# Kernel optimization log

Hardware: AMD Instinct MI355X
Metric: run time of the kernel (lower is better)

## Reference

```python
import jax, jax.numpy as jnp
import numpy as np

K = 3          # kernel_size
N = K * K      # sampling points per pixel
STRIDE = 1
PAD = 1
DIL = 1


def _conv2d(x, w, b):
    # standard NCHW conv for offset / modulation branches
    y = jax.lax.conv_general_dilated(
        x, w, window_strides=(STRIDE, STRIDE),
        padding=((PAD, PAD), (PAD, PAD)),
        rhs_dilation=(DIL, DIL),
        dimension_numbers=('NCHW', 'OIHW', 'NCHW'))
    return y + b[None, :, None, None]


def setup_inputs() -> dict:
    key = jax.random.key(0)
    ks = jax.random.split(key, 6)
    B, C, H, W, O = 8, 64, 96, 96, 64
    x = jax.random.normal(ks[0], (B, C, H, W), jnp.float32)
    # small random offset/modulation weights so sampling points are off-grid
    offset_w = jax.random.normal(ks[1], (2 * N, C, K, K), jnp.float32) * 0.01
    offset_b = jax.random.normal(ks[2], (2 * N,), jnp.float32) * 0.1
    m_w = jax.random.normal(ks[3], (N, C, K, K), jnp.float32) * 0.01
    m_b = jnp.zeros((N,), jnp.float32)
    # Conv3d(in=C, out=O, kernel=(1,1,N)) weight squeezed to [O, C, N]
    conv_w = jax.random.normal(ks[4], (O, C, N), jnp.float32) * (2.0 / (C * N)) ** 0.5
    conv_b = jnp.zeros((O,), jnp.float32)
    return dict(x=x, offset_w=offset_w, offset_b=offset_b,
                m_w=m_w, m_b=m_b, conv_w=conv_w, conv_b=conv_b)


def _deform_forward(x, offset_w, offset_b, m_w, m_b, conv_w, conv_b):
    B, C, H, W = x.shape
    offset = _conv2d(x, offset_w, offset_b)           # [B, 2n, h, w]
    m = jax.nn.sigmoid(_conv2d(x, m_w, m_b))          # [B, n, h, w]
    xp = jnp.pad(x, ((0, 0), (0, 0), (PAD, PAD), (PAD, PAD)))
    Hp, Wp = xp.shape[2], xp.shape[3]
    off = jnp.transpose(offset, (0, 2, 3, 1))         # [B, h, w, 2n]
    mod = jnp.transpose(m, (0, 2, 3, 1))              # [B, h, w, n]

    # p0: conv-center grid on the padded input; pn: kernel-tap offsets
    st = ((K - 1) // 2) * DIL
    p0_x = jnp.arange(st, Hp - (K // 2) * DIL, STRIDE, dtype=jnp.float32)  # [h]
    p0_y = jnp.arange(st, Wp - (K // 2) * DIL, STRIDE, dtype=jnp.float32)  # [w]
    r = jnp.arange(-((K - 1) // 2) * DIL, (K // 2) * DIL + 1, DIL, dtype=jnp.float32)
    pn_x, pn_y = jnp.meshgrid(r, r, indexing='ij')
    pn_x, pn_y = pn_x.reshape(N), pn_y.reshape(N)

    p_x = off[..., :N] + p0_x[None, :, None, None] + pn_x  # [B, h, w, n]
    p_y = off[..., N:] + p0_y[None, None, :, None] + pn_y

    fl_x = jnp.floor(jax.lax.stop_gradient(p_x))
    fl_y = jnp.floor(jax.lax.stop_gradient(p_y))
    q_tl_x = jnp.clip(fl_x, 0, Hp - 1).astype(jnp.int32)
    q_tl_y = jnp.clip(fl_y, 0, Wp - 1).astype(jnp.int32)
    q_br_x = jnp.clip(fl_x + 1, 0, Hp - 1).astype(jnp.int32)
    q_br_y = jnp.clip(fl_y + 1, 0, Wp - 1).astype(jnp.int32)

    pcx = jnp.clip(p_x, 0, Hp - 1)
    pcy = jnp.clip(p_y, 0, Wp - 1)

    tlx = q_tl_x.astype(pcx.dtype); tly = q_tl_y.astype(pcy.dtype)
    brx = q_br_x.astype(pcx.dtype); bry = q_br_y.astype(pcy.dtype)
    g_tl = (1 + (tlx - pcx)) * (1 + (tly - pcy))
    g_tr = (1 + (tlx - pcx)) * (1 - (bry - pcy))
    g_bl = (1 - (brx - pcx)) * (1 + (tly - pcy))
    g_br = (1 - (brx - pcx)) * (1 - (bry - pcy))

    xflat = xp.reshape(B, C, Hp * Wp)

    def gather(qx, qy):
        # per-batch gather: xf [C, Hp*Wp], idx [h, w, n] -> [C, h, w, n]
        return jax.vmap(lambda xf, i: xf[:, i])(xflat, qx * Wp + qy)

    xq_tl = gather(q_tl_x, q_tl_y)
    xq_tr = gather(q_tl_x, q_br_y)
    xq_bl = gather(q_br_x, q_tl_y)
    xq_br = gather(q_br_x, q_br_y)

    x_p = (g_tl[:, None] * xq_tl + g_tr[:, None] * xq_tr +
           g_bl[:, None] * xq_bl + g_br[:, None] * xq_br)
    x_p = x_p * mod[:, None]                           # modulation

    # Conv3d with (1,1,N) kernel == contraction over (C, N)
    out = jnp.einsum('bchwn,ocn->bohw', x_p, conv_w) + conv_b[None, :, None, None]
    return out


def reference(x, offset_w, offset_b, m_w, m_b, conv_w, conv_b):
    return _deform_forward(x, offset_w, offset_b, m_w, m_b, conv_w, conv_b)
```

## Files before the change

### kernel.cpp

```cpp
#include <hip/hip_runtime.h>
#include <hip/hip_fp16.h>
#include <cstddef>

#define B_   8
#define H_   96
#define W_   96
#define HW_  9216
#define PIX_ 73728

#define NWR    9
#define NWC    40
#define WINPX  360
#define NSLOTS 16

typedef __attribute__((ext_vector_type(8))) _Float16 halfx8;
typedef __attribute__((ext_vector_type(2))) __fp16 fp16x2_raw;
typedef __attribute__((ext_vector_type(4))) float floatx4;

#define XT_OFF   0
#define WFM_OFF  (XT_OFF + PIX_*64*2)
#define WFO_OFF  (WFM_OFF + 18*4*64*8*2)

__device__ __forceinline__ unsigned pk2h(float a, float b) {
    fp16x2_raw h = __builtin_amdgcn_cvt_pkrtz(a, b);
    union { fp16x2_raw h2; unsigned u; } t; t.h2 = h; return t.u;
}
__device__ __forceinline__ halfx8 uph8(uint4 u) {
    union { uint4 u4; halfx8 h; } t; t.u4 = u; return t.h;
}
__device__ __forceinline__ halfx8 splat8(unsigned d) {
    union { unsigned u[4]; halfx8 h; } t;
    t.u[0] = d; t.u[1] = d; t.u[2] = d; t.u[3] = d; return t.h;
}

__global__ __launch_bounds__(256) void k_transpose(const float* __restrict__ x,
                                                   unsigned short* __restrict__ xt) {
    __shared__ float tile[64 * 65];
    int bb  = blockIdx.x / 144;
    int sp0 = (blockIdx.x % 144) * 64;
    int t = threadIdx.x;
    int s = t & 63, cg = t >> 6;
    #pragma unroll
    for (int i = 0; i < 16; ++i) {
        int c = cg * 16 + i;
        tile[c * 65 + s] = x[(size_t)(bb * 64 + c) * HW_ + sp0 + s];
    }
    __syncthreads();
    int c8 = t & 7, sgrp = t >> 3;
    #pragma unroll
    for (int i = 0; i < 2; ++i) {
        int s2 = i * 32 + sgrp;
        uint4 pk;
        pk.x = pk2h(tile[(c8 * 8 + 0) * 65 + s2], tile[(c8 * 8 + 1) * 65 + s2]);
        pk.y = pk2h(tile[(c8 * 8 + 2) * 65 + s2], tile[(c8 * 8 + 3) * 65 + s2]);
        pk.z = pk2h(tile[(c8 * 8 + 4) * 65 + s2], tile[(c8 * 8 + 5) * 65 + s2]);
        pk.w = pk2h(tile[(c8 * 8 + 6) * 65 + s2], tile[(c8 * 8 + 7) * 65 + s2]);
        *(uint4*)(xt + (size_t)(bb * HW_ + sp0 + s2) * 64 + c8 * 8) = pk;
    }
}

__global__ __launch_bounds__(256) void k_prepw(const float* __restrict__ offw,
                                               const float* __restrict__ mw,
                                               const float* __restrict__ convw,
                                               unsigned short* __restrict__ wfm,
                                               unsigned short* __restrict__ wfo) {
    int g = blockIdx.x * 256 + threadIdx.x;
    if (g < 4608) {
        int lane = g & 63, mtks = g >> 6;
        int mt = mtks & 3, ks = mtks >> 2;
        int o = mt * 16 + (lane & 15), quad = lane >> 4;
        float v[8];
        #pragma unroll
        for (int j = 0; j < 8; ++j) {
            int k = ks * 32 + quad * 8 + j;
            int t = k / 64, c = k % 64;
            v[j] = convw[(size_t)(o * 64 + c) * 9 + t];
        }
        uint4 pk;
        pk.x = pk2h(v[0], v[1]); pk.y = pk2h(v[2], v[3]);
        pk.z = pk2h(v[4], v[5]); pk.w = pk2h(v[6], v[7]);
        *(uint4*)(wfm + (size_t)g * 8) = pk;
    } else if (g < 4608 + 2304) {
        int g2 = g - 4608;
        int lane = g2 & 63, mtks = g2 >> 6;
        int mt = mtks & 1, ks = mtks >> 1;
        int m = mt * 16 + (lane & 15), quad = lane >> 4;
        float v[8];
        #pragma unroll
        for (int j = 0; j < 8; ++j) {
            int k = ks * 32 + quad * 8 + j;
            int t = k / 64, c = k % 64;
            float f = 0.f;
            if (m < 18)      f = offw[(size_t)(m * 64 + c) * 9 + t];
            else if (m < 27) f = mw[(size_t)((m - 18) * 64 + c) * 9 + t];
            v[j] = f;
        }
        uint4 pk;
        pk.x = pk2h(v[0], v[1]); pk.y = pk2h(v[2], v[3]);
        pk.z = pk2h(v[4], v[5]); pk.w = pk2h(v[6], v[7]);
        *(uint4*)(wfo + (size_t)g2 * 8) = pk;
    }
}

__global__ __launch_bounds__(256, 2) void k_fused(const unsigned short* __restrict__ xt,
                                                  const unsigned short* __restrict__ wfo,
                                                  const unsigned short* __restrict__ wfm,
                                                  const float* __restrict__ offb,
                                                  const float* __restrict__ mb,
                                                  const float* __restrict__ convb,
                                                  float* __restrict__ out) {
    __shared__ __align__(16) unsigned char s_win[(WINPX + NSLOTS) * 128];
    __shared__ float s_off[27 * 66];
    __shared__ __align__(16) unsigned char s_meta[64 * 9 * 16];
    __shared__ int s_cnt;

    int tid = threadIdx.x;
    int w = tid >> 6, lane = tid & 63, col = lane & 15, quad = lane >> 4;
    int blk = blockIdx.x;
    int bb  = blk / 144;
    int rem = blk % 144;
    int hr  = (rem / 3) * 2;
    int wc  = (rem % 3) * 32;
    const unsigned short* xtb = xt + (size_t)bb * HW_ * 64;

    if (tid == 0) s_cnt = 0;
    #pragma unroll
    for (int i = 0; i < 12; ++i) {
        int cid = i * 256 + tid;
        if (cid < WINPX * 8) {
            int p = cid >> 3, ch = cid & 7;
            int wr = p / NWC, wcl = p % NWC;
            int gr = hr - 3 + wr, gc = wc - 4 + wcl;
            uint4 v = make_uint4(0, 0, 0, 0);
            if ((unsigned)gr < 96u && (unsigned)gc < 96u)
                v = *(const uint4*)(xtb + (size_t)(gr * 96 + gc) * 64 + ch * 8);
            *(uint4*)(s_win + (size_t)p * 128 + ((ch ^ (p & 7)) * 16)) = v;
        }
    }
    __syncthreads();

    floatx4 aoff0 = (floatx4){0.f, 0.f, 0.f, 0.f};
    floatx4 aoff1 = (floatx4){0.f, 0.f, 0.f, 0.f};
    {
        int wr_base = 3 + (w >> 1);
        int wc_base = 4 + (w & 1) * 16 + col;
        #pragma unroll
        for (int t = 0; t < 9; ++t) {
            int dh = t / 3 - 1, dw = t % 3 - 1;
            int p = (wr_base + dh) * NWC + (wc_base + dw);
            int pb = p << 7, psw = (p & 7) << 4;
            #pragma unroll
            for (int ksl = 0; ksl < 2; ++ksl) {
                int ks = t * 2 + ksl;
                halfx8 a0 = *(const halfx8*)(wfo + ((size_t)(ks * 2 + 0) * 64 + lane) * 8);
                halfx8 a1 = *(const halfx8*)(wfo + ((size_t)(ks * 2 + 1) * 64 + lane) * 8);
                uint4 bvu = *(const uint4*)(s_win + pb + ((quad * 16 + ksl * 64) ^ psw));
                halfx8 bv = uph8(bvu);
                aoff0 = __builtin_amdgcn_mfma_f32_16x16x32_f16(a0, bv, aoff0, 0, 0, 0);
                aoff1 = __builtin_amdgcn_mfma_f32_16x16x32_f16(a1, bv, aoff1, 0, 0, 0);
            }
        }
    }
    #pragma unroll
    for (int r = 0; r < 4; ++r) {
        s_off[(quad * 4 + r) * 66 + (w * 16 + col)] = aoff0[r];
        int m = 16 + quad * 4 + r;
        if (m < 27) s_off[m * 66 + (w * 16 + col)] = aoff1[r];
    }
    __syncthreads();

    for (int id = tid; id < 576; id += 256) {
        int px = id & 63, n = id >> 6;
        float ox = s_off[n * 66 + px]        + offb[n];
        float oy = s_off[(9 + n) * 66 + px]  + offb[9 + n];
        float mv = s_off[(18 + n) * 66 + px] + mb[n];
        float modv = 1.f / (1.f + __expf(-mv));
        int prow = hr + (px >> 5), pcol = wc + (px & 31);
        float pxx = ox + (float)(prow + 1) + (float)(n / 3 - 1);
        float pyy = oy + (float)(pcol + 1) + (float)(n % 3 - 1);
        float flx = floorf(pxx), fly = floorf(pyy);
        float tlxf = fminf(fmaxf(flx,       0.f), 97.f);
        float tlyf = fminf(fmaxf(fly,       0.f), 97.f);
        float brxf = fminf(fmaxf(flx + 1.f, 0.f), 97.f);
        float bryf = fminf(fmaxf(fly + 1.f, 0.f), 97.f);
        float pcx  = fminf(fmaxf(pxx, 0.f), 97.f);
        float pcy  = fminf(fmaxf(pyy, 0.f), 97.f);
        float gx0 = 1.f + tlxf - pcx;
        float gx1 = 1.f - (brxf - pcx);
        float gy0 = 1.f + tlyf - pcy;
        float gy1 = 1.f - (bryf - pcy);
        int tlx = (int)tlxf, tly = (int)tlyf, brx = (int)brxf, bry = (int)bryf;
        int   qxs[4] = {tlx, tlx, brx, brx};
        int   qys[4] = {tly, bry, tly, bry};
        float gs4[4] = {gx0 * gy0, gx0 * gy1, gx1 * gy0, gx1 * gy1};
        unsigned short si[4]; unsigned short hg[4];
        #pragma unroll
        for (int c4 = 0; c4 < 4; ++c4) {
            int qx = qxs[c4], qy = qys[c4];
            bool valid = (qx >= 1) && (qx <= 96) && (qy >= 1) && (qy <= 96);
            int gr = qx - 1, gc = qy - 1;
            int wr = gr - (hr - 3), wcl = gc - (wc - 4);
            bool inwin = ((unsigned)wr < (unsigned)NWR) && ((unsigned)wcl < (unsigned)NWC);
            unsigned short idxv; float gvf;
            if (inwin) {
                idxv = (unsigned short)(wr * NWC + wcl);
                gvf = gs4[c4] * modv;
            } else if (!valid) {
                idxv = 0; gvf = 0.f;
            } else {
                int s = atomicAdd(&s_cnt, 1);
                int gidx = gr * 96 + gc;
                if (s < NSLOTS) {
                    int ps = WINPX + s;
                    #pragma unroll
                    for (int ch = 0; ch < 8; ++ch) {
                        uint4 v = *(const uint4*)(xtb + (size_t)gidx * 64 + ch * 8);
                        *(uint4*)(s_win + (size_t)ps * 128 + ((ch ^ (ps & 7)) * 16)) = v;
                    }
                    idxv = (unsigned short)ps;
                } else {
                    idxv = (unsigned short)(0x8000u | (unsigned)gidx);
                }
                gvf = gs4[c4] * modv;
            }
            si[c4] = idxv;
            hg[c4] = __half_as_ushort(__float2half_rn(gvf));
        }
        uint4 mw4;
        mw4.x = si[0] | ((unsigned)si[1] << 16);
        mw4.y = si[2] | ((unsigned)si[3] << 16);
        mw4.z = hg[0] | ((unsigned)hg[1] << 16);
        mw4.w = hg[2] | ((unsigned)hg[3] << 16);
        *(uint4*)(s_meta + ((size_t)px * 9 + n) * 16) = mw4;
    }
    __syncthreads();

    int mth = w & 1, pg = w >> 1;
    floatx4 acc[2][2];
    #pragma unroll
    for (int jj = 0; jj < 2; ++jj)
        #pragma unroll
        for (int mtl = 0; mtl < 2; ++mtl) acc[jj][mtl] = (floatx4){0.f, 0.f, 0.f, 0.f};

    int qk0 = quad * 16, qk1 = quad * 16 + 64;

    #pragma unroll
    for (int n = 0; n < 9; ++n) {
        halfx8 af00 = *(const halfx8*)(wfm + ((size_t)((n * 2 + 0) * 4 + mth * 2 + 0) * 64 + lane) * 8);
        halfx8 af01 = *(const halfx8*)(wfm + ((size_t)((n * 2 + 0) * 4 + mth * 2 + 1) * 64 + lane) * 8);
        halfx8 af10 = *(const halfx8*)(wfm + ((size_t)((n * 2 + 1) * 4 + mth * 2 + 0) * 64 + lane) * 8);
        halfx8 af11 = *(const halfx8*)(wfm + ((size_t)((n * 2 + 1) * 4 + mth * 2 + 1) * 64 + lane) * 8);
        #pragma unroll
        for (int jj = 0; jj < 2; ++jj) {
            int px = pg * 32 + jj * 16 + col;
            uint4 mu = *(const uint4*)(s_meta + ((size_t)px * 9 + n) * 16);
            unsigned i0 = mu.x & 0xFFFFu, i1 = mu.x >> 16;
            unsigned i2 = mu.y & 0xFFFFu, i3 = mu.y >> 16;
            int pm0 = (i0 & 0x8000u) ? 0 : (int)i0;
            int pm1 = (i1 & 0x8000u) ? 0 : (int)i1;
            int pm2 = (i2 & 0x8000u) ? 0 : (int)i2;
            int pm3 = (i3 & 0x8000u) ? 0 : (int)i3;
            int b0 = pm0 << 7, s0 = (pm0 & 7) << 4;
            int b1 = pm1 << 7, s1 = (pm1 & 7) << 4;
            int b2 = pm2 << 7, s2 = (pm2 & 7) << 4;
            int b3 = pm3 << 7, s3 = (pm3 & 7) << 4;
            uint4 cA0 = *(const uint4*)(s_win + b0 + (qk0 ^ s0));
            uint4 cA1 = *(const uint4*)(s_win + b1 + (qk0 ^ s1));
            uint4 cA2 = *(const uint4*)(s_win + b2 + (qk0 ^ s2));
            uint4 cA3 = *(const uint4*)(s_win + b3 + (qk0 ^ s3));
            uint4 cB0 = *(const uint4*)(s_win + b0 + (qk1 ^ s0));
            uint4 cB1 = *(const uint4*)(s_win + b1 + (qk1 ^ s1));
            uint4 cB2 = *(const uint4*)(s_win + b2 + (qk1 ^ s2));
            uint4 cB3 = *(const uint4*)(s_win + b3 + (qk1 ^ s3));
            if (__any((int)((i0 | i1 | i2 | i3) & 0x8000u))) {
                if (i0 & 0x8000u) { size_t ga = (size_t)(i0 & 0x3FFFu) * 64 + quad * 8;
                    cA0 = *(const uint4*)(xtb + ga); cB0 = *(const uint4*)(xtb + ga + 32); }
                if (i1 & 0x8000u) { size_t ga = (size_t)(i1 & 0x3FFFu) * 64 + quad * 8;
                    cA1 = *(const uint4*)(xtb + ga); cB1 = *(const uint4*)(xtb + ga + 32); }
                if (i2 & 0x8000u) { size_t ga = (size_t)(i2 & 0x3FFFu) * 64 + quad * 8;
                    cA2 = *(const uint4*)(xtb + ga); cB2 = *(const uint4*)(xtb + ga + 32); }
                if (i3 & 0x8000u) { size_t ga = (size_t)(i3 & 0x3FFFu) * 64 + quad * 8;
                    cA3 = *(const uint4*)(xtb + ga); cB3 = *(const uint4*)(xtb + ga + 32); }
            }
            unsigned gl0 = (mu.z & 0xFFFFu) | (mu.z << 16);
            unsigned gl1 = (mu.z >> 16) | (mu.z & 0xFFFF0000u);
            unsigned gl2 = (mu.w & 0xFFFFu) | (mu.w << 16);
            unsigned gl3 = (mu.w >> 16) | (mu.w & 0xFFFF0000u);
            halfx8 g0 = splat8(gl0), g1 = splat8(gl1), g2 = splat8(gl2), g3 = splat8(gl3);
            halfx8 vA = uph8(cA0) * g0;
            vA += uph8(cA1) * g1; vA += uph8(cA2) * g2; vA += uph8(cA3) * g3;
            halfx8 vB = uph8(cB0) * g0;
            vB += uph8(cB1) * g1; vB += uph8(cB2) * g2; vB += uph8(cB3) * g3;
            acc[jj][0] = __builtin_amdgcn_mfma_f32_16x16x32_f16(af00, vA, acc[jj][0], 0, 0, 0);
            acc[jj][1] = __builtin_amdgcn_mfma_f32_16x16x32_f16(af01, vA, acc[jj][1], 0, 0, 0);
            acc[jj][0] = __builtin_amdgcn_mfma_f32_16x16x32_f16(af10, vB, acc[jj][0], 0, 0, 0);
            acc[jj][1] = __builtin_amdgcn_mfma_f32_16x16x32_f16(af11, vB, acc[jj][1], 0, 0, 0);
        }
    }

    int prow = hr + pg;
    #pragma unroll
    for (int mtl = 0; mtl < 2; ++mtl) {
        float4 cb4 = *(const float4*)&convb[mth * 32 + mtl * 16 + quad * 4];
        #pragma unroll
        for (int jj = 0; jj < 2; ++jj) {
            int sp = prow * 96 + wc + jj * 16 + col;
            #pragma unroll
            for (int r = 0; r < 4; ++r) {
                int o = mth * 32 + mtl * 16 + quad * 4 + r;
                float bias = (r == 0) ? cb4.x : (r == 1) ? cb4.y : (r == 2) ? cb4.z : cb4.w;
                out[(size_t)(bb * 64 + o) * HW_ + sp] = acc[jj][mtl][r] + bias;
            }
        }
    }
}

extern "C" void kernel_launch(void* const* d_in, const int* in_sizes, int n_in,
                              void* d_out, int out_size, void* d_ws, size_t ws_size,
                              hipStream_t stream) {
    const float* x     = (const float*)d_in[0];
    const float* offw  = (const float*)d_in[1];
    const float* offb  = (const float*)d_in[2];
    const float* mw    = (const float*)d_in[3];
    const float* mb    = (const float*)d_in[4];
    const float* convw = (const float*)d_in[5];
    const float* convb = (const float*)d_in[6];
    char* ws = (char*)d_ws;
    unsigned short* xt16 = (unsigned short*)(ws + XT_OFF);
    unsigned short* wfm  = (unsigned short*)(ws + WFM_OFF);
    unsigned short* wfo  = (unsigned short*)(ws + WFO_OFF);
    float* out = (float*)d_out;

    k_transpose<<<dim3(1152), dim3(256), 0, stream>>>(x, xt16);
    k_prepw    <<<dim3(27),   dim3(256), 0, stream>>>(offw, mw, convw, wfm, wfo);
    k_fused    <<<dim3(1152), dim3(256), 0, stream>>>(xt16, wfo, wfm, offb, mb, convb, out);
}
```

Before: 126.1 us.

## Merge weight prep into transpose launch, vectorize loads, async window load to LDS

Folds the weight-packing kernel into extra blocks of the transpose kernel, removing one launch. The transpose now reads x with float4 loads. The fused kernel's halo-window fill uses global_load_lds direct-to-LDS loads with clamped addresses, then zeroes out-of-bounds pixels in a second pass. The async path relies on the LDS write layout of global_load_lds matching the swizzled layout, and the extra pass adds a barrier.

Result: faster. 120.2 us (-4.7%).

```diff
diff --git a/kernel.cpp b/kernel.cpp
--- a/kernel.cpp
+++ b/kernel.cpp
@@ -32,18 +32,72 @@
     union { unsigned u[4]; halfx8 h; } t;
     t.u[0] = d; t.u[1] = d; t.u[2] = d; t.u[3] = d; return t.h;
 }
+__device__ __forceinline__ void async_ld16(const void* g, void* l) {
+    __builtin_amdgcn_global_load_lds((const __attribute__((address_space(1))) void*)g,
+                                     (__attribute__((address_space(3))) void*)l,
+                                     16, 0, 0);
+}
 
 __global__ __launch_bounds__(256) void k_transpose(const float* __restrict__ x,
-                                                   unsigned short* __restrict__ xt) {
+                                                   unsigned short* __restrict__ xt,
+                                                   const float* __restrict__ offw,
+                                                   const float* __restrict__ mw,
+                                                   const float* __restrict__ convw,
+                                                   unsigned short* __restrict__ wfm,
+                                                   unsigned short* __restrict__ wfo) {
+    if (blockIdx.x >= 1152) {
+        int g = (blockIdx.x - 1152) * 256 + threadIdx.x;
+        if (g < 4608) {
+            int lane = g & 63, mtks = g >> 6;
+            int mt = mtks & 3, ks = mtks >> 2;
+            int o = mt * 16 + (lane & 15), quad = lane >> 4;
+            float v[8];
+            #pragma unroll
+            for (int j = 0; j < 8; ++j) {
+                int k = ks * 32 + quad * 8 + j;
+                int t = k / 64, c = k % 64;
+                v[j] = convw[(size_t)(o * 64 + c) * 9 + t];
+            }
+            uint4 pk;
+            pk.x = pk2h(v[0], v[1]); pk.y = pk2h(v[2], v[3]);
+            pk.z = pk2h(v[4], v[5]); pk.w = pk2h(v[6], v[7]);
+            *(uint4*)(wfm + (size_t)g * 8) = pk;
+        } else if (g < 4608 + 2304) {
+            int g2 = g - 4608;
+            int lane = g2 & 63, mtks = g2 >> 6;
+            int mt = mtks & 1, ks = mtks >> 1;
+            int m = mt * 16 + (lane & 15), quad = lane >> 4;
+            float v[8];
+            #pragma unroll
+            for (int j = 0; j < 8; ++j) {
+                int k = ks * 32 + quad * 8 + j;
+                int t = k / 64, c = k % 64;
+                float f = 0.f;
+                if (m < 18)      f = offw[(size_t)(m * 64 + c) * 9 + t];
+                else if (m < 27) f = mw[(size_t)((m - 18) * 64 + c) * 9 + t];
+                v[j] = f;
+            }
+            uint4 pk;
+            pk.x = pk2h(v[0], v[1]); pk.y = pk2h(v[2], v[3]);
+            pk.z = pk2h(v[4], v[5]); pk.w = pk2h(v[6], v[7]);
+            *(uint4*)(wfo + (size_t)g2 * 8) = pk;
+        }
+        return;
+    }
+
     __shared__ float tile[64 * 65];
     int bb  = blockIdx.x / 144;
     int sp0 = (blockIdx.x % 144) * 64;
     int t = threadIdx.x;
-    int s = t & 63, cg = t >> 6;
-    #pragma unroll
-    for (int i = 0; i < 16; ++i) {
-        int c = cg * 16 + i;
-        tile[c * 65 + s] = x[(size_t)(bb * 64 + c) * HW_ + sp0 + s];
+    int s4 = (t & 15) * 4, cq = t >> 4;
+    #pragma unroll
+    for (int i = 0; i < 4; ++i) {
+        int c = cq + 16 * i;
+        float4 v = *(const float4*)&x[(size_t)(bb * 64 + c) * HW_ + sp0 + s4];
+        tile[c * 65 + s4 + 0] = v.x;
+        tile[c * 65 + s4 + 1] = v.y;
+        tile[c * 65 + s4 + 2] = v.z;
+        tile[c * 65 + s4 + 3] = v.w;
     }
     __syncthreads();
     int c8 = t & 7, sgrp = t >> 3;
@@ -56,49 +110,6 @@
         pk.z = pk2h(tile[(c8 * 8 + 4) * 65 + s2], tile[(c8 * 8 + 5) * 65 + s2]);
         pk.w = pk2h(tile[(c8 * 8 + 6) * 65 + s2], tile[(c8 * 8 + 7) * 65 + s2]);
         *(uint4*)(xt + (size_t)(bb * HW_ + sp0 + s2) * 64 + c8 * 8) = pk;
-    }
-}
-
-__global__ __launch_bounds__(256) void k_prepw(const float* __restrict__ offw,
-                                               const float* __restrict__ mw,
-                                               const float* __restrict__ convw,
-                                               unsigned short* __restrict__ wfm,
-                                               unsigned short* __restrict__ wfo) {
-    int g = blockIdx.x * 256 + threadIdx.x;
-    if (g < 4608) {
-        int lane = g & 63, mtks = g >> 6;
-        int mt = mtks & 3, ks = mtks >> 2;
-        int o = mt * 16 + (lane & 15), quad = lane >> 4;
-        float v[8];
-        #pragma unroll
-        for (int j = 0; j < 8; ++j) {
-            int k = ks * 32 + quad * 8 + j;
-            int t = k / 64, c = k % 64;
-            v[j] = convw[(size_t)(o * 64 + c) * 9 + t];
-        }
-        uint4 pk;
-        pk.x = pk2h(v[0], v[1]); pk.y = pk2h(v[2], v[3]);
-        pk.z = pk2h(v[4], v[5]); pk.w = pk2h(v[6], v[7]);
-        *(uint4*)(wfm + (size_t)g * 8) = pk;
-    } else if (g < 4608 + 2304) {
-        int g2 = g - 4608;
-        int lane = g2 & 63, mtks = g2 >> 6;
-        int mt = mtks & 1, ks = mtks >> 1;
-        int m = mt * 16 + (lane & 15), quad = lane >> 4;
-        float v[8];
-        #pragma unroll
-        for (int j = 0; j < 8; ++j) {
-            int k = ks * 32 + quad * 8 + j;
-            int t = k / 64, c = k % 64;
-            float f = 0.f;
-            if (m < 18)      f = offw[(size_t)(m * 64 + c) * 9 + t];
-            else if (m < 27) f = mw[(size_t)((m - 18) * 64 + c) * 9 + t];
-            v[j] = f;
-        }
-        uint4 pk;
-        pk.x = pk2h(v[0], v[1]); pk.y = pk2h(v[2], v[3]);
-        pk.z = pk2h(v[4], v[5]); pk.w = pk2h(v[6], v[7]);
-        *(uint4*)(wfo + (size_t)g2 * 8) = pk;
     }
 }
 
@@ -124,17 +135,27 @@
     const unsigned short* xtb = xt + (size_t)bb * HW_ * 64;
 
     if (tid == 0) s_cnt = 0;
-    #pragma unroll
-    for (int i = 0; i < 12; ++i) {
-        int cid = i * 256 + tid;
-        if (cid < WINPX * 8) {
-            int p = cid >> 3, ch = cid & 7;
-            int wr = p / NWC, wcl = p % NWC;
+    {
+        int p0  = lane >> 3;
+        int cgx = (lane & 7) ^ p0;
+        for (int i = w; i < 45; i += 4) {
+            int p = i * 8 + p0;
+            int wr = p / NWC, wcl = p - wr * NWC;
             int gr = hr - 3 + wr, gc = wc - 4 + wcl;
-            uint4 v = make_uint4(0, 0, 0, 0);
-            if ((unsigned)gr < 96u && (unsigned)gc < 96u)
-                v = *(const uint4*)(xtb + (size_t)(gr * 96 + gc) * 64 + ch * 8);
-            *(uint4*)(s_win + (size_t)p * 128 + ((ch ^ (p & 7)) * 16)) = v;
+            int grc = min(max(gr, 0), 95), gcc = min(max(gc, 0), 95);
+            const unsigned short* src = xtb + ((size_t)(grc * 96 + gcc) * 64 + cgx * 8);
+            async_ld16(src, s_win + i * 1024);
+        }
+    }
+    __syncthreads();
+    for (int p = tid; p < WINPX; p += 256) {
+        int wr = p / NWC, wcl = p - wr * NWC;
+        int gr = hr - 3 + wr, gc = wc - 4 + wcl;
+        if ((unsigned)gr >= 96u || (unsigned)gc >= 96u) {
+            uint4 z = make_uint4(0, 0, 0, 0);
+            #pragma unroll
+            for (int cg = 0; cg < 8; ++cg)
+                *(uint4*)(s_win + p * 128 + cg * 16) = z;
         }
     }
     __syncthreads();
@@ -331,7 +352,6 @@
     unsigned short* wfo  = (unsigned short*)(ws + WFO_OFF);
     float* out = (float*)d_out;
 
-    k_transpose<<<dim3(1152), dim3(256), 0, stream>>>(x, xt16);
-    k_prepw    <<<dim3(27),   dim3(256), 0, stream>>>(offw, mw, convw, wfm, wfo);
-    k_fused    <<<dim3(1152), dim3(256), 0, stream>>>(xt16, wfo, wfm, offb, mb, convb, out);
-}
+    k_transpose<<<dim3(1152 + 27), dim3(256), 0, stream>>>(x, xt16, offw, mw, convw, wfm, wfo);
+    k_fused    <<<dim3(1152),      dim3(256), 0, stream>>>(xt16, wfo, wfm, offb, mb, convb, out);
+}
```
